# Performance work log

Hardware: AMD Instinct MI355X
Metric: run time of the kernel (lower is better)

## Reference

```python
import jax, jax.numpy as jnp
import numpy as np

C = 256
R = 16
K = 7


def setup_inputs() -> dict:
    key = jax.random.key(0)
    k1, k2, k3, k4 = jax.random.split(key, 4)
    x = jax.random.normal(k1, (32, C, 64, 64), dtype=jnp.float32)
    # mlp: Conv2d(C, C//R, 1, bias=False) then Conv2d(C//R, C, 1, bias=False)
    w1 = jax.random.normal(k2, (C // R, C), dtype=jnp.float32) * (1.0 / np.sqrt(C))
    w2 = jax.random.normal(k3, (C, C // R), dtype=jnp.float32) * (1.0 / np.sqrt(C // R))
    # conv_spatial: Conv2d(2, 1, 7, padding=3, bias=False) -> OIHW [1,2,7,7]
    w_sp = jax.random.normal(k4, (1, 2, K, K), dtype=jnp.float32) * (1.0 / np.sqrt(2 * K * K))
    return {"x": x, "w1": w1, "w2": w2, "w_sp": w_sp}


def _cbam(x, w1, w2, w_sp):
    B, Cc, H, W = x.shape
    # --- channel attention ---
    avg = jnp.mean(x, axis=(2, 3))            # [B, C]
    mx = jnp.max(x, axis=(2, 3))              # [B, C]

    def mlp(v):
        h = jax.nn.relu(jnp.einsum('bc,rc->br', v, w1))  # [B, C//R]
        return jnp.einsum('br,cr->bc', h, w2)            # [B, C]

    ch_att = jax.nn.sigmoid(mlp(avg) + mlp(mx))          # [B, C]
    x = x * ch_att[:, :, None, None]

    # --- spatial attention ---
    avg_sp = jnp.mean(x, axis=1, keepdims=True)          # [B,1,H,W]
    max_sp = jnp.max(x, axis=1, keepdims=True)           # [B,1,H,W]
    sp = jnp.concatenate([avg_sp, max_sp], axis=1)       # [B,2,H,W]
    att = jax.lax.conv_general_dilated(
        sp, w_sp, window_strides=(1, 1), padding='SAME',
        dimension_numbers=('NCHW', 'OIHW', 'NCHW'))      # [B,1,H,W]
    return x * jax.nn.sigmoid(att)


def reference(x, w1, w2, w_sp):
    return _cbam(x, w1, w2, w_sp)
```

## Files before the change

kernel.cpp:

```cpp
#include <hip/hip_runtime.h>
#include <math.h>

#define Bn 32
#define Cn 256
#define Hn 64
#define Wn 64
#define HWn 4096
#define CRn 16

__device__ __forceinline__ float sigmoidf_(float v) { return 1.0f / (1.0f + __expf(-v)); }

__global__ __launch_bounds__(256) void k_chanstats(const float* __restrict__ x,
                                                   float* __restrict__ avg,
                                                   float* __restrict__ mx) {
    int bc = blockIdx.x;
    const float4* xv = (const float4*)(x + (size_t)bc * HWn);
    int t = threadIdx.x;
    float s = 0.0f, m = -INFINITY;
#pragma unroll
    for (int j = 0; j < 4; ++j) {
        float4 v = xv[t + j * 256];
        s += v.x + v.y + v.z + v.w;
        m = fmaxf(m, fmaxf(fmaxf(v.x, v.y), fmaxf(v.z, v.w)));
    }
#pragma unroll
    for (int off = 32; off > 0; off >>= 1) {
        s += __shfl_down(s, off);
        m = fmaxf(m, __shfl_down(m, off));
    }
    __shared__ float ss[4], sm[4];
    int wave = t >> 6, lane = t & 63;
    if (lane == 0) { ss[wave] = s; sm[wave] = m; }
    __syncthreads();
    if (t == 0) {
        s = ss[0] + ss[1] + ss[2] + ss[3];
        m = fmaxf(fmaxf(sm[0], sm[1]), fmaxf(sm[2], sm[3]));
        avg[bc] = s * (1.0f / HWn);
        mx[bc]  = m;
    }
}

__global__ __launch_bounds__(256) void k_mlp(const float* __restrict__ avg,
                                             const float* __restrict__ mx,
                                             const float* __restrict__ w1,
                                             const float* __restrict__ w2,
                                             float* __restrict__ ch_att) {
    int b = blockIdx.x;
    int t = threadIdx.x;
    __shared__ float sv[2][Cn];
    __shared__ float part[32][8];
    __shared__ float h[32];
    sv[0][t] = avg[b * Cn + t];
    sv[1][t] = mx[b * Cn + t];
    __syncthreads();
    int d  = t & 31;
    int ch = t >> 5;
    int r  = d & 15;
    const float* v = sv[d >> 4];
    const float* wrow = w1 + r * Cn + ch * 32;
    float acc = 0.0f;
#pragma unroll
    for (int c = 0; c < 32; ++c) acc += v[ch * 32 + c] * wrow[c];
    part[d][ch] = acc;
    __syncthreads();
    if (t < 32) {
        float a = 0.0f;
#pragma unroll
        for (int k = 0; k < 8; ++k) a += part[t][k];
        h[t] = fmaxf(a, 0.0f);
    }
    __syncthreads();
    float acc2 = 0.0f;
#pragma unroll
    for (int rr = 0; rr < CRn; ++rr) acc2 += (h[rr] + h[CRn + rr]) * w2[t * CRn + rr];
    ch_att[b * Cn + t] = sigmoidf_(acc2);
}

__global__ __launch_bounds__(256) void k_spstats(const float* __restrict__ x,
                                                 const float* __restrict__ ch_att,
                                                 float* __restrict__ avg_sp,
                                                 float* __restrict__ max_sp) {
    int blk = blockIdx.x;
    int b = blk >> 6;
    int seg = blk & 63;
    int t = threadIdx.x;
    int f4 = t & 15;
    int cg = t >> 4;

    __shared__ float satt[Cn];
    satt[t] = ch_att[b * Cn + t];
    __syncthreads();

    const float* xb = x + ((size_t)b * Cn) * HWn + seg * 64;
    float4 s = {0.f, 0.f, 0.f, 0.f};
    float4 m = {-INFINITY, -INFINITY, -INFINITY, -INFINITY};
#pragma unroll
    for (int i = 0; i < 16; ++i) {
        int c = (i << 4) + cg;
        float4 v = ((const float4*)(xb + (size_t)c * HWn))[f4];
        float a = satt[c];
        v.x *= a; v.y *= a; v.z *= a; v.w *= a;
        s.x += v.x; s.y += v.y; s.z += v.z; s.w += v.w;
        m.x = fmaxf(m.x, v.x); m.y = fmaxf(m.y, v.y);
        m.z = fmaxf(m.z, v.z); m.w = fmaxf(m.w, v.w);
    }
#pragma unroll
    for (int off = 32; off >= 16; off >>= 1) {
        s.x += __shfl_down(s.x, off); s.y += __shfl_down(s.y, off);
        s.z += __shfl_down(s.z, off); s.w += __shfl_down(s.w, off);
        m.x = fmaxf(m.x, __shfl_down(m.x, off));
        m.y = fmaxf(m.y, __shfl_down(m.y, off));
        m.z = fmaxf(m.z, __shfl_down(m.z, off));
        m.w = fmaxf(m.w, __shfl_down(m.w, off));
    }
    __shared__ float4 ps[4][16], pm[4][16];
    int wave = t >> 6, lane = t & 63;
    if (lane < 16) { ps[wave][lane] = s; pm[wave][lane] = m; }
    __syncthreads();
    if (t < 16) {
        s = ps[0][t]; m = pm[0][t];
#pragma unroll
        for (int g = 1; g < 4; ++g) {
            float4 os = ps[g][t], om = pm[g][t];
            s.x += os.x; s.y += os.y; s.z += os.z; s.w += os.w;
            m.x = fmaxf(m.x, om.x); m.y = fmaxf(m.y, om.y);
            m.z = fmaxf(m.z, om.z); m.w = fmaxf(m.w, om.w);
        }
        const float inv = 1.0f / Cn;
        float4 av = {s.x * inv, s.y * inv, s.z * inv, s.w * inv};
        ((float4*)(avg_sp + b * HWn + seg * 64))[t] = av;
        ((float4*)(max_sp + b * HWn + seg * 64))[t] = m;
    }
}

__global__ __launch_bounds__(256) void k_convfinal(const float* __restrict__ x,
                                                   const float* __restrict__ ch_att,
                                                   const float* __restrict__ avg_sp,
                                                   const float* __restrict__ max_sp,
                                                   const float* __restrict__ w_sp,
                                                   float* __restrict__ out) {
    int blk = blockIdx.x;
    int b = blk >> 5;
    int y0 = (blk & 31) << 1;
    int t = threadIdx.x;

    __shared__ float ca[Cn];
    __shared__ float wk[98];
    __shared__ float ha[8][64];
    __shared__ float hm[8][64];
    __shared__ float att2[128];

    ca[t] = ch_att[b * Cn + t];
    if (t < 98) wk[t] = w_sp[t];
    const float* ab = avg_sp + b * HWn;
    const float* mb = max_sp + b * HWn;
#pragma unroll
    for (int k = 0; k < 4; ++k) {
        int idx = k * 256 + t;
        int mapi = idx >> 9;
        int r = (idx >> 6) & 7;
        int col = idx & 63;
        int y = y0 - 3 + r;
        float v = 0.0f;
        if (y >= 0 && y < Hn) v = (mapi == 0 ? ab : mb)[y * Wn + col];
        if (mapi == 0) ha[r][col] = v; else hm[r][col] = v;
    }
    __syncthreads();

    if (t < 128) {
        int row = t >> 6;
        int col = t & 63;
        float acc = 0.0f;
#pragma unroll
        for (int ky = 0; ky < 7; ++ky) {
            int hr = row + ky;
#pragma unroll
            for (int kx = 0; kx < 7; ++kx) {
                int xc = col + kx - 3;
                if (xc < 0 || xc >= Wn) continue;
                acc += ha[hr][xc] * wk[ky * 7 + kx] + hm[hr][xc] * wk[49 + ky * 7 + kx];
            }
        }
        att2[t] = sigmoidf_(acc);
    }
    __syncthreads();

    int f4 = t & 31;
    int cg = t >> 5;
    float4 a4 = ((const float4*)att2)[f4];
    size_t base = ((size_t)b * Cn) * HWn + (size_t)y0 * Wn;
    const float* xb = x + base;
    float* ob = out + base;
#pragma unroll 4
    for (int i = 0; i < 32; ++i) {
        int c = (i << 3) + cg;
        size_t off = (size_t)c * HWn;
        float4 v = ((const float4*)(xb + off))[f4];
        float sfac = ca[c];
        float4 rv;
        rv.x = v.x * sfac * a4.x;
        rv.y = v.y * sfac * a4.y;
        rv.z = v.z * sfac * a4.z;
        rv.w = v.w * sfac * a4.w;
        ((float4*)(ob + off))[f4] = rv;
    }
}

extern "C" void kernel_launch(void* const* d_in, const int* in_sizes, int n_in,
                              void* d_out, int out_size, void* d_ws, size_t ws_size,
                              hipStream_t stream) {
    const float* x    = (const float*)d_in[0];
    const float* w1   = (const float*)d_in[1];
    const float* w2   = (const float*)d_in[2];
    const float* w_sp = (const float*)d_in[3];
    float* out = (float*)d_out;

    float* ws = (float*)d_ws;
    float* avg    = ws;
    float* mx     = avg + Bn * Cn;
    float* ch_att = mx + Bn * Cn;
    float* avg_sp = ch_att + Bn * Cn;
    float* max_sp = avg_sp + Bn * HWn;

    k_chanstats<<<Bn * Cn, 256, 0, stream>>>(x, avg, mx);
    k_mlp<<<Bn, 256, 0, stream>>>(avg, mx, w1, w2, ch_att);
    k_spstats<<<Bn * 64, 256, 0, stream>>>(x, ch_att, avg_sp, max_sp);
    k_convfinal<<<Bn * 32, 256, 0, stream>>>(x, ch_att, avg_sp, max_sp, w_sp, out);
}
```

Measured before the change: 289.4 us.

## Fuse channel MLP into spatial-stats kernel and retile final conv kernel per row

Removes the separate MLP launch by having every spatial-stats block recompute the small channel-attention MLP redundantly, with segment 0 writing the result for later use. The final kernel now handles one output row per block (twice as many blocks), splits the 7x7 conv across all 256 threads with a partial-sum reduction, and issues the first four x loads before the conv barrier so they overlap the attention computation. The trade-off is redundant MLP work and weight reads in 2048 blocks, plus more blocks that each reload conv halo rows.

Result: faster. 277.4 us (-4.1%).

```diff
diff --git a/kernel.cpp b/kernel.cpp
--- a/kernel.cpp
+++ b/kernel.cpp
@@ -40,57 +40,57 @@
     }
 }
 
-__global__ __launch_bounds__(256) void k_mlp(const float* __restrict__ avg,
-                                             const float* __restrict__ mx,
-                                             const float* __restrict__ w1,
-                                             const float* __restrict__ w2,
-                                             float* __restrict__ ch_att) {
-    int b = blockIdx.x;
-    int t = threadIdx.x;
-    __shared__ float sv[2][Cn];
-    __shared__ float part[32][8];
-    __shared__ float h[32];
-    sv[0][t] = avg[b * Cn + t];
-    sv[1][t] = mx[b * Cn + t];
-    __syncthreads();
-    int d  = t & 31;
-    int ch = t >> 5;
-    int r  = d & 15;
-    const float* v = sv[d >> 4];
-    const float* wrow = w1 + r * Cn + ch * 32;
-    float acc = 0.0f;
-#pragma unroll
-    for (int c = 0; c < 32; ++c) acc += v[ch * 32 + c] * wrow[c];
-    part[d][ch] = acc;
-    __syncthreads();
-    if (t < 32) {
-        float a = 0.0f;
-#pragma unroll
-        for (int k = 0; k < 8; ++k) a += part[t][k];
-        h[t] = fmaxf(a, 0.0f);
-    }
-    __syncthreads();
-    float acc2 = 0.0f;
-#pragma unroll
-    for (int rr = 0; rr < CRn; ++rr) acc2 += (h[rr] + h[CRn + rr]) * w2[t * CRn + rr];
-    ch_att[b * Cn + t] = sigmoidf_(acc2);
-}
-
 __global__ __launch_bounds__(256) void k_spstats(const float* __restrict__ x,
-                                                 const float* __restrict__ ch_att,
+                                                 const float* __restrict__ avg,
+                                                 const float* __restrict__ mx,
+                                                 const float* __restrict__ w1,
+                                                 const float* __restrict__ w2,
+                                                 float* __restrict__ ch_att,
                                                  float* __restrict__ avg_sp,
                                                  float* __restrict__ max_sp) {
     int blk = blockIdx.x;
     int b = blk >> 6;
     int seg = blk & 63;
     int t = threadIdx.x;
+
+    __shared__ float sv[2][Cn];
+    __shared__ float part[32][8];
+    __shared__ float h[32];
+    __shared__ float satt[Cn];
+    sv[0][t] = avg[b * Cn + t];
+    sv[1][t] = mx[b * Cn + t];
+    __syncthreads();
+    {
+        int d  = t & 31;
+        int chk = t >> 5;
+        int r  = d & 15;
+        const float* v = sv[d >> 4];
+        const float* wrow = w1 + r * Cn + chk * 32;
+        float acc = 0.0f;
+#pragma unroll
+        for (int c = 0; c < 32; ++c) acc += v[chk * 32 + c] * wrow[c];
+        part[d][chk] = acc;
+    }
+    __syncthreads();
+    if (t < 32) {
+        float a = 0.0f;
+#pragma unroll
+        for (int k = 0; k < 8; ++k) a += part[t][k];
+        h[t] = fmaxf(a, 0.0f);
+    }
+    __syncthreads();
+    {
+        float a2 = 0.0f;
+#pragma unroll
+        for (int rr = 0; rr < CRn; ++rr) a2 += (h[rr] + h[CRn + rr]) * w2[t * CRn + rr];
+        float catt = sigmoidf_(a2);
+        satt[t] = catt;
+        if (seg == 0) ch_att[b * Cn + t] = catt;
+    }
+    __syncthreads();
+
     int f4 = t & 15;
     int cg = t >> 4;
-
-    __shared__ float satt[Cn];
-    satt[t] = ch_att[b * Cn + t];
-    __syncthreads();
-
     const float* xb = x + ((size_t)b * Cn) * HWn + seg * 64;
     float4 s = {0.f, 0.f, 0.f, 0.f};
     float4 m = {-INFINITY, -INFINITY, -INFINITY, -INFINITY};
@@ -140,15 +140,16 @@
                                                    const float* __restrict__ w_sp,
                                                    float* __restrict__ out) {
     int blk = blockIdx.x;
-    int b = blk >> 5;
-    int y0 = (blk & 31) << 1;
+    int b = blk >> 6;
+    int y0 = blk & 63;
     int t = threadIdx.x;
 
     __shared__ float ca[Cn];
     __shared__ float wk[98];
-    __shared__ float ha[8][64];
-    __shared__ float hm[8][64];
-    __shared__ float att2[128];
+    __shared__ float ha[7][64];
+    __shared__ float hm[7][64];
+    __shared__ float cpart[4][64];
+    __shared__ float att1[64];
 
     ca[t] = ch_att[b * Cn + t];
     if (t < 98) wk[t] = w_sp[t];
@@ -157,51 +158,69 @@
 #pragma unroll
     for (int k = 0; k < 4; ++k) {
         int idx = k * 256 + t;
-        int mapi = idx >> 9;
-        int r = (idx >> 6) & 7;
-        int col = idx & 63;
-        int y = y0 - 3 + r;
-        float v = 0.0f;
-        if (y >= 0 && y < Hn) v = (mapi == 0 ? ab : mb)[y * Wn + col];
-        if (mapi == 0) ha[r][col] = v; else hm[r][col] = v;
-    }
-    __syncthreads();
-
-    if (t < 128) {
-        int row = t >> 6;
-        int col = t & 63;
-        float acc = 0.0f;
-#pragma unroll
-        for (int ky = 0; ky < 7; ++ky) {
-            int hr = row + ky;
-#pragma unroll
-            for (int kx = 0; kx < 7; ++kx) {
-                int xc = col + kx - 3;
-                if (xc < 0 || xc >= Wn) continue;
-                acc += ha[hr][xc] * wk[ky * 7 + kx] + hm[hr][xc] * wk[49 + ky * 7 + kx];
-            }
+        if (idx < 896) {
+            int mapi = idx >= 448;
+            int j = mapi ? idx - 448 : idx;
+            int rr = j >> 6;
+            int col = j & 63;
+            int y = y0 - 3 + rr;
+            float vv = 0.0f;
+            if (y >= 0 && y < Hn) vv = (mapi ? mb : ab)[y * Wn + col];
+            if (mapi) hm[rr][col] = vv; else ha[rr][col] = vv;
         }
-        att2[t] = sigmoidf_(acc);
-    }
-    __syncthreads();
-
-    int f4 = t & 31;
-    int cg = t >> 5;
-    float4 a4 = ((const float4*)att2)[f4];
+    }
+
+    int f4 = t & 15;
+    int cg = t >> 4;
     size_t base = ((size_t)b * Cn) * HWn + (size_t)y0 * Wn;
     const float* xb = x + base;
     float* ob = out + base;
-#pragma unroll 4
-    for (int i = 0; i < 32; ++i) {
-        int c = (i << 3) + cg;
+    float4 p0 = ((const float4*)(xb + (size_t)(cg) * HWn))[f4];
+    float4 p1 = ((const float4*)(xb + (size_t)(16 + cg) * HWn))[f4];
+    float4 p2 = ((const float4*)(xb + (size_t)(32 + cg) * HWn))[f4];
+    float4 p3 = ((const float4*)(xb + (size_t)(48 + cg) * HWn))[f4];
+
+    __syncthreads();
+
+    {
+        int col = t & 63;
+        int pr = t >> 6;
+        float acc = 0.0f;
+#pragma unroll
+        for (int kk = 0; kk < 2; ++kk) {
+            int ky = pr * 2 + kk;
+            if (ky < 7) {
+#pragma unroll
+                for (int kx = 0; kx < 7; ++kx) {
+                    int xc = col + kx - 3;
+                    if (xc < 0 || xc >= Wn) continue;
+                    acc += ha[ky][xc] * wk[ky * 7 + kx] + hm[ky][xc] * wk[49 + ky * 7 + kx];
+                }
+            }
+        }
+        cpart[pr][col] = acc;
+    }
+    __syncthreads();
+    if (t < 64) att1[t] = sigmoidf_(cpart[0][t] + cpart[1][t] + cpart[2][t] + cpart[3][t]);
+    __syncthreads();
+
+    float4 a4 = ((const float4*)att1)[f4];
+#pragma unroll
+    for (int i = 0; i < 16; ++i) {
+        int c = (i << 4) + cg;
         size_t off = (size_t)c * HWn;
-        float4 v = ((const float4*)(xb + off))[f4];
-        float sfac = ca[c];
+        float4 v;
+        if (i == 0) v = p0;
+        else if (i == 1) v = p1;
+        else if (i == 2) v = p2;
+        else if (i == 3) v = p3;
+        else v = ((const float4*)(xb + off))[f4];
+        float sf = ca[c];
         float4 rv;
-        rv.x = v.x * sfac * a4.x;
-        rv.y = v.y * sfac * a4.y;
-        rv.z = v.z * sfac * a4.z;
-        rv.w = v.w * sfac * a4.w;
+        rv.x = v.x * sf * a4.x;
+        rv.y = v.y * sf * a4.y;
+        rv.z = v.z * sf * a4.z;
+        rv.w = v.w * sf * a4.w;
         ((float4*)(ob + off))[f4] = rv;
     }
 }
@@ -223,7 +242,6 @@
     float* max_sp = avg_sp + Bn * HWn;
 
     k_chanstats<<<Bn * Cn, 256, 0, stream>>>(x, avg, mx);
-    k_mlp<<<Bn, 256, 0, stream>>>(avg, mx, w1, w2, ch_att);
-    k_spstats<<<Bn * 64, 256, 0, stream>>>(x, ch_att, avg_sp, max_sp);
-    k_convfinal<<<Bn * 32, 256, 0, stream>>>(x, ch_att, avg_sp, max_sp, w_sp, out);
-}
+    k_spstats<<<Bn * 64, 256, 0, stream>>>(x, avg, mx, w1, w2, ch_att, avg_sp, max_sp);
+    k_convfinal<<<Bn * Hn, 256, 0, stream>>>(x, ch_att, avg_sp, max_sp, w_sp, out);
+}
```
